# Kernel optimization log

Measured on AMD Instinct MI355X. Metric: run time of the kernel, lower is better.

Reference implementation:

```python
import jax, jax.numpy as jnp
import numpy as np

NEG_INIT = -1.0e9


def setup_inputs() -> dict:
    key = jax.random.key(0)
    k1, k2, k3, k4, k5, k6, k7 = jax.random.split(key, 7)
    N, D, d_att, G = 262144, 512, 128, 512
    feats = jax.random.normal(k1, (N, D), dtype=jnp.float32)
    index = jnp.sort(jax.random.randint(k2, (N,), 0, G, dtype=jnp.int64))
    # torch Linear params: weight (out,in), bias (out,)
    Vw = jax.random.normal(k3, (d_att, D), dtype=jnp.float32) / np.sqrt(D)
    Vb = jax.random.normal(k4, (d_att,), dtype=jnp.float32) * 0.01
    Uw = jax.random.normal(k5, (d_att, D), dtype=jnp.float32) / np.sqrt(D)
    Ub = jax.random.normal(k6, (d_att,), dtype=jnp.float32) * 0.01
    ww = jax.random.normal(k7, (1, d_att), dtype=jnp.float32) / np.sqrt(d_att)
    return {"feats": feats, "index": index, "num_groups": G,
            "Vw": Vw, "Vb": Vb, "Uw": Uw, "Ub": Ub, "ww": ww}


def reference(feats, index, num_groups, Vw, Vb, Uw, Ub, ww):
    # gated attention MLP: A = tanh(V x) * sigmoid(U x); scores = w A
    A = jnp.tanh(feats @ Vw.T + Vb) * jax.nn.sigmoid(feats @ Uw.T + Ub)  # (N, d_att)
    scores = (A @ ww.T)[:, 0]  # (N,)
    # segment max with -1e9 init (matches scatter_reduce amax include_self)
    max_per_group = jax.ops.segment_max(scores, index, num_segments=num_groups)
    max_per_group = jnp.maximum(max_per_group, NEG_INIT)  # empty segments -> -1e9
    exp_scores = jnp.exp(scores - max_per_group[index])
    denom = jax.ops.segment_sum(exp_scores, index, num_segments=num_groups)
    weights = exp_scores / (denom[index] + 1e-8)
    # weighted scatter-sum pooling: (num_groups, D)
    out = jax.ops.segment_sum(feats * weights[:, None], index, num_segments=num_groups)
    return out
```

## Files before the change

kernel.cpp:

```cpp
#include <hip/hip_runtime.h>
#include <hip/hip_fp8.h>
#include <cstddef>

#define NEG_INIT -1.0e9f

typedef _Float16 f16x8 __attribute__((ext_vector_type(8)));
typedef _Float16 f16x4 __attribute__((ext_vector_type(4)));
typedef _Float16 f16x2 __attribute__((ext_vector_type(2)));
typedef float f32x4 __attribute__((ext_vector_type(4)));

constexpr int D   = 512;
constexpr int BM  = 32;
constexpr int BK  = 32;
constexpr int NKS = D / BK;
constexpr int SSK = 4;
constexpr int NSS = NKS / SSK;
constexpr int LDH  = 520;
constexpr int LDRB = 520;
constexpr int PS  = 516;
constexpr float RSC  = 2048.f;
constexpr float RISC = 1.f / 2048.f;

#define BAR_LGKM()                                            \
    do {                                                      \
        asm volatile("s_waitcnt lgkmcnt(0)" ::: "memory");    \
        __builtin_amdgcn_s_barrier();                         \
        asm volatile("" ::: "memory");                        \
    } while (0)

#if __has_builtin(__builtin_amdgcn_cvt_pk_fp8_f32) && __has_builtin(__builtin_amdgcn_cvt_f32_fp8)
#define HW_FP8 1
#else
#define HW_FP8 0
#endif

__device__ __forceinline__ unsigned int pack_fp8x4(float r0, float r1,
                                                   float r2, float r3) {
#if HW_FP8
    int p = __builtin_amdgcn_cvt_pk_fp8_f32(r0, r1, 0, false);
    p     = __builtin_amdgcn_cvt_pk_fp8_f32(r2, r3, p, true);
    return (unsigned int)p;
#else
    __hip_fp8_e4m3 q0(r0), q1(r1), q2(r2), q3(r3);
    return (unsigned int)q0.__x | ((unsigned int)q1.__x << 8) |
           ((unsigned int)q2.__x << 16) | ((unsigned int)q3.__x << 24);
#endif
}

template <int SEL>
__device__ __forceinline__ float unpack_fp8(unsigned int word) {
#if HW_FP8
    return __builtin_amdgcn_cvt_f32_fp8((int)word, SEL);
#else
    __hip_fp8_e4m3 q;
    q.__x = (unsigned char)(word >> (8 * SEL));
    return (float)q;
#endif
}

__device__ __forceinline__ float fast_tanh(float v) {
    float e2 = __expf(2.f * v);
    return 1.f - 2.f * __builtin_amdgcn_rcpf(e2 + 1.f);
}
__device__ __forceinline__ float fast_sigmoid(float u) {
    return __builtin_amdgcn_rcpf(1.f + __expf(-u));
}

__global__ __launch_bounds__(64) void k_wprep(const float* __restrict__ Vw,
                                              const float* __restrict__ Uw,
                                              _Float16* __restrict__ Wfrag) {
    const int bid  = blockIdx.x;
    const int lane = threadIdx.x;
    const int j    = bid & 3;
    const int ks   = (bid >> 2) & 15;
    const int wc   = bid >> 6;
    const int l15  = lane & 15;
    const int kgrp = lane >> 4;
    const float* src = (j < 2 ? Vw + (size_t)(wc * 32 + j * 16 + l15) * D
                              : Uw + (size_t)(wc * 32 + (j - 2) * 16 + l15) * D)
                       + ks * BK + kgrp * 8;
    f16x8 h;
    #pragma unroll
    for (int e = 0; e < 8; ++e) h[e] = (_Float16)src[e];
    *(f16x8*)(Wfrag + ((size_t)bid * 64 + lane) * 8) = h;
}

__global__ __launch_bounds__(256) void k_bounds(const int* __restrict__ index,
                                                int N, int G,
                                                int* __restrict__ start) {
    int g = blockIdx.x * blockDim.x + threadIdx.x;
    if (g > G) return;
    int lo = 0, hi = N;
    while (lo < hi) {
        int mid = (lo + hi) >> 1;
        if (index[mid] < g) lo = mid + 1; else hi = mid;
    }
    start[g] = lo;
}

__global__ __launch_bounds__(512, 6) void k_fused(
    const float* __restrict__ feats, const _Float16* __restrict__ Wfrag,
    const float* __restrict__ Vb, const float* __restrict__ Ub,
    const float* __restrict__ ww, const int* __restrict__ index,
    const int* __restrict__ start, float* __restrict__ P, int N)
{
    __shared__ __align__(16) _Float16 Xh[BM][LDH];
    __shared__ __align__(8)  unsigned char Xr8[BM * LDRB];
    __shared__ float sred[8][BM];
    __shared__ float srow[BM];
    __shared__ float evals[BM];

    const int t    = threadIdx.x;
    const int lane = t & 63;
    const int wc   = t >> 6;
    const int l15  = lane & 15;
    const int kgrp = lane >> 4;
    const int blk  = blockIdx.x;
    const int rb   = blk * BM;

    const int srw  = t >> 4;
    const int scol = (t & 15) * 8;
    const float* xg = feats + (size_t)(rb + srw) * D + scol;

    float4 xa[2][2];
    auto issueX = [&](int ss) {
        const float* p = xg + ss * 128;
        xa[ss & 1][0] = *(const float4*)p;
        xa[ss & 1][1] = *(const float4*)(p + 4);
    };
    auto commitX = [&](int ss) {
        const int c0 = ss * 128 + scol;
        float v[8];
        v[0] = xa[ss & 1][0].x; v[1] = xa[ss & 1][0].y;
        v[2] = xa[ss & 1][0].z; v[3] = xa[ss & 1][0].w;
        v[4] = xa[ss & 1][1].x; v[5] = xa[ss & 1][1].y;
        v[6] = xa[ss & 1][1].z; v[7] = xa[ss & 1][1].w;
        f16x8 h;
        float res[8];
        #pragma unroll
        for (int e = 0; e < 8; ++e) {
            h[e] = (_Float16)v[e];
            res[e] = (v[e] - (float)h[e]) * RSC;
        }
        unsigned int rp0 = pack_fp8x4(res[0], res[1], res[2], res[3]);
        unsigned int rp1 = pack_fp8x4(res[4], res[5], res[6], res[7]);
        *(f16x8*)&Xh[srw][c0] = h;
        uint2 rw = {rp0, rp1};
        *(uint2*)&Xr8[srw * LDRB + c0] = rw;
    };

    const _Float16* wbV = Wfrag + (size_t)(wc >> 1) * 32768
                                + (size_t)(wc & 1) * 512 + (size_t)lane * 8;
    const _Float16* wbU = wbV + 1024;

    f32x4 accV[2], accU[2];
    #pragma unroll
    for (int i = 0; i < 2; ++i) {
        accV[i] = (f32x4){0.f, 0.f, 0.f, 0.f};
        accU[i] = (f32x4){0.f, 0.f, 0.f, 0.f};
    }

    issueX(0); issueX(1);
    commitX(0);
    BAR_LGKM();

    #pragma unroll
    for (int ss = 0; ss < NSS; ++ss) {
        if (ss + 2 < NSS) issueX(ss + 2);
        #pragma unroll
        for (int k2 = 0; k2 < SSK; ++k2) {
            const int ks = ss * SSK + k2;
            f16x8 bv = *(const f16x8*)(wbV + (size_t)ks * 2048);
            f16x8 bu = *(const f16x8*)(wbU + (size_t)ks * 2048);
            f16x8 ha[2];
            #pragma unroll
            for (int i = 0; i < 2; ++i)
                ha[i] = *(const f16x8*)&Xh[i * 16 + l15][ks * BK + kgrp * 8];
            #pragma unroll
            for (int i = 0; i < 2; ++i) {
                accV[i] = __builtin_amdgcn_mfma_f32_16x16x32_f16(ha[i], bv, accV[i], 0, 0, 0);
                accU[i] = __builtin_amdgcn_mfma_f32_16x16x32_f16(ha[i], bu, accU[i], 0, 0, 0);
            }
        }
        if (ss + 1 < NSS) {
            commitX(ss + 1);
            BAR_LGKM();
        }
    }

    {
        const int c = wc * 16 + l15;
        const float vb = Vb[c], ub = Ub[c], w = ww[c];
        float part[2][4];
        #pragma unroll
        for (int i = 0; i < 2; ++i)
            #pragma unroll
            for (int r = 0; r < 4; ++r) {
                float v = accV[i][r] + vb;
                float u = accU[i][r] + ub;
                part[i][r] = w * fast_tanh(v) * fast_sigmoid(u);
            }
        #pragma unroll
        for (int off = 1; off < 16; off <<= 1)
            #pragma unroll
            for (int i = 0; i < 2; ++i)
                #pragma unroll
                for (int r = 0; r < 4; ++r)
                    part[i][r] += __shfl_xor(part[i][r], off);
        if (l15 == 0) {
            #pragma unroll
            for (int i = 0; i < 2; ++i)
                #pragma unroll
                for (int r = 0; r < 4; ++r)
                    sred[wc][i * 16 + kgrp * 4 + r] = part[i][r];
        }
    }
    __syncthreads();
    if (t < BM) {
        float s = sred[0][t];
        #pragma unroll
        for (int w8 = 1; w8 < 8; ++w8) s += sred[w8][t];
        srow[t] = s;
    }
    __syncthreads();

    const int gl = index[rb];
    const int gh = index[rb + BM - 1];
    for (int g = gl + wc; g <= gh; g += 8) {
        const int r0 = max(start[g], rb), r1 = min(start[g + 1], rb + BM);
        if (r1 <= r0) continue;
        const bool in = (lane >= r0 - rb) && (lane < r1 - rb);
        float m = in ? srow[lane] : NEG_INIT;
        #pragma unroll
        for (int off = 32; off; off >>= 1) m = fmaxf(m, __shfl_xor(m, off));
        float e = in ? expf(srow[lane] - m) : 0.f;
        if (in) evals[lane] = e;
        float s = e;
        #pragma unroll
        for (int off = 32; off; off >>= 1) s += __shfl_xor(s, off);
        if (lane == 0) {
            float* slot = P + (size_t)(blk + g) * PS;
            slot[0] = m; slot[1] = s;
        }
    }
    __syncthreads();

    if (t < 256) {
        const int c0 = t * 2;
        for (int g = gl; g <= gh; ++g) {
            const int r0 = max(start[g], rb), r1 = min(start[g + 1], rb + BM);
            if (r1 <= r0) continue;
            float a0 = 0.f, a1 = 0.f;
            for (int r = r0; r < r1; ++r) {
                const int rr = r - rb;
                const float e = evals[rr];
                f16x2 hp = *(const f16x2*)&Xh[rr][c0];
                unsigned int rv = *(const unsigned short*)&Xr8[rr * LDRB + c0];
                float x0 = fmaf(unpack_fp8<0>(rv), RISC, (float)hp[0]);
                float x1 = fmaf(unpack_fp8<1>(rv), RISC, (float)hp[1]);
                a0 = fmaf(e, x0, a0);
                a1 = fmaf(e, x1, a1);
            }
            float2 o = {a0, a1};
            *(float2*)(P + (size_t)(blk + g) * PS + 4 + c0) = o;
        }
    }
}

__global__ __launch_bounds__(512) void k_merge(const float* __restrict__ P,
                                               const int* __restrict__ start,
                                               float* __restrict__ out)
{
    const int g = blockIdx.x, t = threadIdx.x;
    const int s0 = start[g], s1 = start[g + 1];
    if (s0 >= s1) { out[(size_t)g * D + t] = 0.f; return; }
    const int b0 = s0 >> 5, b1 = (s1 - 1) >> 5;
    float M = NEG_INIT;
    for (int b = b0; b <= b1; ++b)
        M = fmaxf(M, P[(size_t)(b + g) * PS]);
    float den = 0.f, acc = 0.f;
    for (int b = b0; b <= b1; ++b) {
        const float* slot = P + (size_t)(b + g) * PS;
        float w = expf(slot[0] - M);
        den += w * slot[1];
        acc += w * slot[4 + t];
    }
    out[(size_t)g * D + t] = acc / (den + 1e-8f);
}

extern "C" void kernel_launch(void* const* d_in, const int* in_sizes, int n_in,
                              void* d_out, int out_size, void* d_ws, size_t ws_size,
                              hipStream_t stream) {
    const float* feats = (const float*)d_in[0];
    const int*   index = (const int*)d_in[1];
    const float* Vw = (const float*)d_in[3];
    const float* Vb = (const float*)d_in[4];
    const float* Uw = (const float*)d_in[5];
    const float* Ub = (const float*)d_in[6];
    const float* ww = (const float*)d_in[7];
    float* out = (float*)d_out;

    const int N = in_sizes[1];
    const int G = out_size / D;
    const int nblk = (N + BM - 1) / BM;

    _Float16* Wfrag = (_Float16*)d_ws;
    int* start      = (int*)(Wfrag + (size_t)256 * 512);
    size_t off      = (size_t)256 * 512 * 2 + (G + 1) * 4;
    off             = (off + 15) & ~(size_t)15;
    float* P        = (float*)((char*)d_ws + off);

    hipLaunchKernelGGL(k_wprep, dim3(256), dim3(64), 0, stream, Vw, Uw, Wfrag);
    hipLaunchKernelGGL(k_bounds, dim3((G + 1 + 255) / 256), dim3(256), 0, stream,
                       index, N, G, start);
    hipLaunchKernelGGL(k_fused, dim3(nblk), dim3(512), 0, stream,
                       feats, Wfrag, Vb, Ub, ww, index, start, P, N);
    hipLaunchKernelGGL(k_merge, dim3(G), dim3(512), 0, stream, P, start, out);
}
```

Baseline: 206.6 us.

## Double row tile to 64 and use 1024-thread blocks with 2D wave split

The fused kernel's row tile grows from 32 to 64 rows, with 1024-thread blocks whose 16 waves split into 4 row groups by 4 column groups. Each wave now loads four weight fragments per k-step and reuses one activation fragment across them, so weight fetches per row drop. The pooling stage now gives each thread one column instead of two, and the merge kernel's partial-slot indexing follows the new tile size. The larger tile roughly doubles LDS use per block, which likely cuts resident waves per CU and may hurt latency hiding in this memory-bound kernel.

```diff
diff --git a/kernel.cpp b/kernel.cpp
--- a/kernel.cpp
+++ b/kernel.cpp
@@ -10,7 +10,7 @@
 typedef float f32x4 __attribute__((ext_vector_type(4)));
 
 constexpr int D   = 512;
-constexpr int BM  = 32;
+constexpr int BM  = 64;
 constexpr int BK  = 32;
 constexpr int NKS = D / BK;
 constexpr int SSK = 4;
@@ -98,7 +98,7 @@
     start[g] = lo;
 }
 
-__global__ __launch_bounds__(512, 6) void k_fused(
+__global__ __launch_bounds__(1024, 4) void k_fused(
     const float* __restrict__ feats, const _Float16* __restrict__ Wfrag,
     const float* __restrict__ Vb, const float* __restrict__ Ub,
     const float* __restrict__ ww, const int* __restrict__ index,
@@ -106,13 +106,15 @@
 {
     __shared__ __align__(16) _Float16 Xh[BM][LDH];
     __shared__ __align__(8)  unsigned char Xr8[BM * LDRB];
-    __shared__ float sred[8][BM];
+    __shared__ float sred[4][BM];
     __shared__ float srow[BM];
     __shared__ float evals[BM];
 
     const int t    = threadIdx.x;
     const int lane = t & 63;
-    const int wc   = t >> 6;
+    const int wv   = t >> 6;
+    const int rg   = wv >> 2;
+    const int cg   = wv & 3;
     const int l15  = lane & 15;
     const int kgrp = lane >> 4;
     const int blk  = blockIdx.x;
@@ -149,9 +151,7 @@
         *(uint2*)&Xr8[srw * LDRB + c0] = rw;
     };
 
-    const _Float16* wbV = Wfrag + (size_t)(wc >> 1) * 32768
-                                + (size_t)(wc & 1) * 512 + (size_t)lane * 8;
-    const _Float16* wbU = wbV + 1024;
+    const _Float16* wb = Wfrag + (size_t)cg * 32768 + (size_t)lane * 8;
 
     f32x4 accV[2], accU[2];
     #pragma unroll
@@ -170,17 +170,16 @@
         #pragma unroll
         for (int k2 = 0; k2 < SSK; ++k2) {
             const int ks = ss * SSK + k2;
-            f16x8 bv = *(const f16x8*)(wbV + (size_t)ks * 2048);
-            f16x8 bu = *(const f16x8*)(wbU + (size_t)ks * 2048);
-            f16x8 ha[2];
-            #pragma unroll
-            for (int i = 0; i < 2; ++i)
-                ha[i] = *(const f16x8*)&Xh[i * 16 + l15][ks * BK + kgrp * 8];
-            #pragma unroll
-            for (int i = 0; i < 2; ++i) {
-                accV[i] = __builtin_amdgcn_mfma_f32_16x16x32_f16(ha[i], bv, accV[i], 0, 0, 0);
-                accU[i] = __builtin_amdgcn_mfma_f32_16x16x32_f16(ha[i], bu, accU[i], 0, 0, 0);
-            }
+            const _Float16* wk = wb + (size_t)ks * 2048;
+            f16x8 bv0 = *(const f16x8*)(wk);
+            f16x8 bv1 = *(const f16x8*)(wk + 512);
+            f16x8 bu0 = *(const f16x8*)(wk + 1024);
+            f16x8 bu1 = *(const f16x8*)(wk + 1536);
+            f16x8 ha = *(const f16x8*)&Xh[rg * 16 + l15][ks * BK + kgrp * 8];
+            accV[0] = __builtin_amdgcn_mfma_f32_16x16x32_f16(ha, bv0, accV[0], 0, 0, 0);
+            accV[1] = __builtin_amdgcn_mfma_f32_16x16x32_f16(ha, bv1, accV[1], 0, 0, 0);
+            accU[0] = __builtin_amdgcn_mfma_f32_16x16x32_f16(ha, bu0, accU[0], 0, 0, 0);
+            accU[1] = __builtin_amdgcn_mfma_f32_16x16x32_f16(ha, bu1, accU[1], 0, 0, 0);
         }
         if (ss + 1 < NSS) {
             commitX(ss + 1);
@@ -189,44 +188,39 @@
     }
 
     {
-        const int c = wc * 16 + l15;
-        const float vb = Vb[c], ub = Ub[c], w = ww[c];
         float part[2][4];
         #pragma unroll
-        for (int i = 0; i < 2; ++i)
+        for (int j = 0; j < 2; ++j) {
+            const int c = cg * 32 + j * 16 + l15;
+            const float vb = Vb[c], ub = Ub[c], w = ww[c];
             #pragma unroll
             for (int r = 0; r < 4; ++r) {
-                float v = accV[i][r] + vb;
-                float u = accU[i][r] + ub;
-                part[i][r] = w * fast_tanh(v) * fast_sigmoid(u);
+                float v = accV[j][r] + vb;
+                float u = accU[j][r] + ub;
+                part[j][r] = w * fast_tanh(v) * fast_sigmoid(u);
             }
+        }
         #pragma unroll
         for (int off = 1; off < 16; off <<= 1)
             #pragma unroll
-            for (int i = 0; i < 2; ++i)
+            for (int j = 0; j < 2; ++j)
                 #pragma unroll
                 for (int r = 0; r < 4; ++r)
-                    part[i][r] += __shfl_xor(part[i][r], off);
+                    part[j][r] += __shfl_xor(part[j][r], off);
         if (l15 == 0) {
             #pragma unroll
-            for (int i = 0; i < 2; ++i)
-                #pragma unroll
-                for (int r = 0; r < 4; ++r)
-                    sred[wc][i * 16 + kgrp * 4 + r] = part[i][r];
+            for (int r = 0; r < 4; ++r)
+                sred[cg][rg * 16 + kgrp * 4 + r] = part[0][r] + part[1][r];
         }
     }
     __syncthreads();
-    if (t < BM) {
-        float s = sred[0][t];
-        #pragma unroll
-        for (int w8 = 1; w8 < 8; ++w8) s += sred[w8][t];
-        srow[t] = s;
-    }
+    if (t < BM)
+        srow[t] = sred[0][t] + sred[1][t] + sred[2][t] + sred[3][t];
     __syncthreads();
 
     const int gl = index[rb];
     const int gh = index[rb + BM - 1];
-    for (int g = gl + wc; g <= gh; g += 8) {
+    for (int g = gl + wv; g <= gh; g += 16) {
         const int r0 = max(start[g], rb), r1 = min(start[g + 1], rb + BM);
         if (r1 <= r0) continue;
         const bool in = (lane >= r0 - rb) && (lane < r1 - rb);
@@ -245,24 +239,20 @@
     }
     __syncthreads();
 
-    if (t < 256) {
-        const int c0 = t * 2;
+    if (t < 512) {
+        const int c0 = t;
         for (int g = gl; g <= gh; ++g) {
             const int r0 = max(start[g], rb), r1 = min(start[g + 1], rb + BM);
             if (r1 <= r0) continue;
-            float a0 = 0.f, a1 = 0.f;
+            float a = 0.f;
             for (int r = r0; r < r1; ++r) {
                 const int rr = r - rb;
-                const float e = evals[rr];
-                f16x2 hp = *(const f16x2*)&Xh[rr][c0];
-                unsigned int rv = *(const unsigned short*)&Xr8[rr * LDRB + c0];
-                float x0 = fmaf(unpack_fp8<0>(rv), RISC, (float)hp[0]);
-                float x1 = fmaf(unpack_fp8<1>(rv), RISC, (float)hp[1]);
-                a0 = fmaf(e, x0, a0);
-                a1 = fmaf(e, x1, a1);
+                float h = (float)Xh[rr][c0];
+                unsigned int rv = Xr8[rr * LDRB + c0];
+                float x = fmaf(unpack_fp8<0>(rv), RISC, h);
+                a = fmaf(evals[rr], x, a);
             }
-            float2 o = {a0, a1};
-            *(float2*)(P + (size_t)(blk + g) * PS + 4 + c0) = o;
+            P[(size_t)(blk + g) * PS + 4 + c0] = a;
         }
     }
 }
@@ -274,7 +264,7 @@
     const int g = blockIdx.x, t = threadIdx.x;
     const int s0 = start[g], s1 = start[g + 1];
     if (s0 >= s1) { out[(size_t)g * D + t] = 0.f; return; }
-    const int b0 = s0 >> 5, b1 = (s1 - 1) >> 5;
+    const int b0 = s0 >> 6, b1 = (s1 - 1) >> 6;
     float M = NEG_INIT;
     for (int b = b0; b <= b1; ++b)
         M = fmaxf(M, P[(size_t)(b + g) * PS]);
@@ -313,7 +303,7 @@
     hipLaunchKernelGGL(k_wprep, dim3(256), dim3(64), 0, stream, Vw, Uw, Wfrag);
     hipLaunchKernelGGL(k_bounds, dim3((G + 1 + 255) / 256), dim3(256), 0, stream,
                        index, N, G, start);
-    hipLaunchKernelGGL(k_fused, dim3(nblk), dim3(512), 0, stream,
+    hipLaunchKernelGGL(k_fused, dim3(nblk), dim3(1024), 0, stream,
                        feats, Wfrag, Vb, Ub, ww, index, start, P, N);
     hipLaunchKernelGGL(k_merge, dim3(G), dim3(512), 0, stream, P, start, out);
 }
```

Result: slower. 322.2 us (+56.0%).

## Drop fp8 residual LDS copy; re-read fp32 feats from global for pooling

Applied to the files above, without the earlier changes.

Removes the fp16+fp8-residual reconstruction of the input tile held in shared memory. The pooling stage now re-reads the exact fp32 features from global memory, which should mostly hit in cache since the block just streamed them. This frees the residual LDS buffer and the conversion work in commitX, and the occupancy hint is raised from 6 to 8. The cost is a second global read of each row during pooling, which adds memory traffic if those reads miss cache.

```diff
diff --git a/kernel.cpp b/kernel.cpp
--- a/kernel.cpp
+++ b/kernel.cpp
@@ -1,12 +1,10 @@
 #include <hip/hip_runtime.h>
-#include <hip/hip_fp8.h>
 #include <cstddef>
 
 #define NEG_INIT -1.0e9f
 
 typedef _Float16 f16x8 __attribute__((ext_vector_type(8)));
 typedef _Float16 f16x4 __attribute__((ext_vector_type(4)));
-typedef _Float16 f16x2 __attribute__((ext_vector_type(2)));
 typedef float f32x4 __attribute__((ext_vector_type(4)));
 
 constexpr int D   = 512;
@@ -15,11 +13,8 @@
 constexpr int NKS = D / BK;
 constexpr int SSK = 4;
 constexpr int NSS = NKS / SSK;
-constexpr int LDH  = 520;
-constexpr int LDRB = 520;
+constexpr int LDH = 520;
 constexpr int PS  = 516;
-constexpr float RSC  = 2048.f;
-constexpr float RISC = 1.f / 2048.f;
 
 #define BAR_LGKM()                                            \
     do {                                                      \
@@ -27,36 +22,6 @@
         __builtin_amdgcn_s_barrier();                         \
         asm volatile("" ::: "memory");                        \
     } while (0)
-
-#if __has_builtin(__builtin_amdgcn_cvt_pk_fp8_f32) && __has_builtin(__builtin_amdgcn_cvt_f32_fp8)
-#define HW_FP8 1
-#else
-#define HW_FP8 0
-#endif
-
-__device__ __forceinline__ unsigned int pack_fp8x4(float r0, float r1,
-                                                   float r2, float r3) {
-#if HW_FP8
-    int p = __builtin_amdgcn_cvt_pk_fp8_f32(r0, r1, 0, false);
-    p     = __builtin_amdgcn_cvt_pk_fp8_f32(r2, r3, p, true);
-    return (unsigned int)p;
-#else
-    __hip_fp8_e4m3 q0(r0), q1(r1), q2(r2), q3(r3);
-    return (unsigned int)q0.__x | ((unsigned int)q1.__x << 8) |
-           ((unsigned int)q2.__x << 16) | ((unsigned int)q3.__x << 24);
-#endif
-}
-
-template <int SEL>
-__device__ __forceinline__ float unpack_fp8(unsigned int word) {
-#if HW_FP8
-    return __builtin_amdgcn_cvt_f32_fp8((int)word, SEL);
-#else
-    __hip_fp8_e4m3 q;
-    q.__x = (unsigned char)(word >> (8 * SEL));
-    return (float)q;
-#endif
-}
 
 __device__ __forceinline__ float fast_tanh(float v) {
     float e2 = __expf(2.f * v);
@@ -98,14 +63,13 @@
     start[g] = lo;
 }
 
-__global__ __launch_bounds__(512, 6) void k_fused(
+__global__ __launch_bounds__(512, 8) void k_fused(
     const float* __restrict__ feats, const _Float16* __restrict__ Wfrag,
     const float* __restrict__ Vb, const float* __restrict__ Ub,
     const float* __restrict__ ww, const int* __restrict__ index,
     const int* __restrict__ start, float* __restrict__ P, int N)
 {
     __shared__ __align__(16) _Float16 Xh[BM][LDH];
-    __shared__ __align__(8)  unsigned char Xr8[BM * LDRB];
     __shared__ float sred[8][BM];
     __shared__ float srow[BM];
     __shared__ float evals[BM];
@@ -130,23 +94,10 @@
     };
     auto commitX = [&](int ss) {
         const int c0 = ss * 128 + scol;
-        float v[8];
-        v[0] = xa[ss & 1][0].x; v[1] = xa[ss & 1][0].y;
-        v[2] = xa[ss & 1][0].z; v[3] = xa[ss & 1][0].w;
-        v[4] = xa[ss & 1][1].x; v[5] = xa[ss & 1][1].y;
-        v[6] = xa[ss & 1][1].z; v[7] = xa[ss & 1][1].w;
-        f16x8 h;
-        float res[8];
-        #pragma unroll
-        for (int e = 0; e < 8; ++e) {
-            h[e] = (_Float16)v[e];
-            res[e] = (v[e] - (float)h[e]) * RSC;
-        }
-        unsigned int rp0 = pack_fp8x4(res[0], res[1], res[2], res[3]);
-        unsigned int rp1 = pack_fp8x4(res[4], res[5], res[6], res[7]);
+        float4 a = xa[ss & 1][0], b = xa[ss & 1][1];
+        f16x8 h = { (_Float16)a.x, (_Float16)a.y, (_Float16)a.z, (_Float16)a.w,
+                    (_Float16)b.x, (_Float16)b.y, (_Float16)b.z, (_Float16)b.w };
         *(f16x8*)&Xh[srw][c0] = h;
-        uint2 rw = {rp0, rp1};
-        *(uint2*)&Xr8[srw * LDRB + c0] = rw;
     };
 
     const _Float16* wbV = Wfrag + (size_t)(wc >> 1) * 32768
@@ -252,14 +203,10 @@
             if (r1 <= r0) continue;
             float a0 = 0.f, a1 = 0.f;
             for (int r = r0; r < r1; ++r) {
-                const int rr = r - rb;
-                const float e = evals[rr];
-                f16x2 hp = *(const f16x2*)&Xh[rr][c0];
-                unsigned int rv = *(const unsigned short*)&Xr8[rr * LDRB + c0];
-                float x0 = fmaf(unpack_fp8<0>(rv), RISC, (float)hp[0]);
-                float x1 = fmaf(unpack_fp8<1>(rv), RISC, (float)hp[1]);
-                a0 = fmaf(e, x0, a0);
-                a1 = fmaf(e, x1, a1);
+                const float e = evals[r - rb];
+                float2 x = *(const float2*)(feats + (size_t)r * D + c0);
+                a0 = fmaf(e, x.x, a0);
+                a1 = fmaf(e, x.y, a1);
             }
             float2 o = {a0, a1};
             *(float2*)(P + (size_t)(blk + g) * PS + 4 + c0) = o;
```

Measured after the change: 266.3 us. 28.9% more time.
